# Kernel tuning notes

Measured on AMD Instinct MI355X. Metric: run time of the kernel, lower is better.

## Reference

```python
import jax, jax.numpy as jnp
import numpy as np

N_HEAD = 16


def setup_inputs() -> dict:
    key = jax.random.key(0)
    k1, k2, k3 = jax.random.split(key, 3)
    B, T, C = 4, 2048, 1024
    x = jax.random.normal(k1, (B, T, C), dtype=jnp.float32)
    W = jax.random.normal(k2, (3 * C, C), dtype=jnp.float32) * (1.0 / np.sqrt(C))
    b = jax.random.normal(k3, (3 * C,), dtype=jnp.float32) * 0.02
    return {"x": x, "W": W, "b": b, "input_pos": 0}


def reference(x, W, b, input_pos):
    # cache=False path; input_pos is unused (kept for signature fidelity).
    B, T, C = x.shape
    H = N_HEAD
    hs = C // H
    # Fused QKV projection: torch Linear is x @ W.T + b -> [B, T, 3C]
    qkv = (jnp.einsum('btc,oc->bto', x, W) + b).reshape(B, T, 3, H, hs)
    # q, k, v: [B, H, T, hs]
    q = jnp.transpose(qkv[:, :, 0], (0, 2, 1, 3))
    k = jnp.transpose(qkv[:, :, 1], (0, 2, 1, 3))
    v = jnp.transpose(qkv[:, :, 2], (0, 2, 1, 3))
    scale = hs ** (-0.5)
    # scores: [B, H, T, T]
    scores = jnp.einsum('bhqd,bhkd->bhqk', q, k) * scale
    causal = jnp.tril(jnp.ones((T, T), dtype=bool))
    scores = jnp.where(causal, scores, -jnp.inf)
    wei = jax.nn.softmax(scores, axis=-1)
    out = jnp.einsum('bhqk,bhkd->bhqd', wei, v)  # [B, H, T, hs]
    return jnp.transpose(out, (0, 2, 1, 3)).reshape(B, T, C)
```

## Files before the change

### kernel.cpp

```cpp
#include <hip/hip_runtime.h>
#include <stdint.h>

using s16x8 = __attribute__((ext_vector_type(8))) short;
using u16x8 = __attribute__((ext_vector_type(8))) unsigned short;
using f32x4 = __attribute__((ext_vector_type(4))) float;

#define NEG_INF (-__builtin_inff())

__device__ __forceinline__ unsigned short f2bf(float f) {
    union { float f; uint32_t u; } v; v.f = f;
    uint32_t u = (v.u + 0x7FFFu + ((v.u >> 16) & 1u)) >> 16;
    return (unsigned short)u;
}

__device__ __forceinline__ f32x4 zero4() { f32x4 z = {0.f, 0.f, 0.f, 0.f}; return z; }

__device__ __forceinline__ void async16(const void* g, void* l) {
    __builtin_amdgcn_global_load_lds(
        reinterpret_cast<const uint32_t __attribute__((address_space(1)))*>(
            reinterpret_cast<uintptr_t>(g)),
        reinterpret_cast<uint32_t __attribute__((address_space(3)))*>(
            (uint32_t)reinterpret_cast<uintptr_t>(l)),
        16, 0, 0);
}

__global__ void cvt_bf16(const float* __restrict__ in, unsigned short* __restrict__ out, int n) {
    int i = (blockIdx.x * 256 + threadIdx.x) * 8;
    if (i >= n) return;
    f32x4 a = *(const f32x4*)(in + i);
    f32x4 c = *(const f32x4*)(in + i + 4);
    u16x8 o;
    o[0] = f2bf(a[0]); o[1] = f2bf(a[1]); o[2] = f2bf(a[2]); o[3] = f2bf(a[3]);
    o[4] = f2bf(c[0]); o[5] = f2bf(c[1]); o[6] = f2bf(c[2]); o[7] = f2bf(c[3]);
    *(u16x8*)(out + i) = o;
}

__global__ __launch_bounds__(256, 2)
void qkv_gemm(const unsigned short* __restrict__ A,
              const unsigned short* __restrict__ Bw,
              const float* __restrict__ bias,
              unsigned short* __restrict__ Qo,
              unsigned short* __restrict__ Ko,
              unsigned short* __restrict__ Vto) {
    constexpr int Kd = 1024, T = 2048, H = 16;
    __shared__ __align__(16) unsigned short As[128 * 64];
    __shared__ __align__(16) unsigned short Bs[128 * 64];
    const int tid = threadIdx.x;
    const int wave = tid >> 6, lane = tid & 63;
    const int q4 = lane >> 4, l15 = lane & 15;
    const int bm = blockIdx.y * 128, bn = blockIdx.x * 128;
    const int wm = (wave >> 1) * 64, wn = (wave & 1) * 64;

    f32x4 acc[4][4];
#pragma unroll
    for (int a = 0; a < 4; ++a)
#pragma unroll
        for (int c = 0; c < 4; ++c) acc[a][c] = zero4();

    for (int k0 = 0; k0 < Kd; k0 += 64) {
#pragma unroll
        for (int r = 0; r < 4; ++r) {
            int u = r * 256 + tid;
            int row = u >> 3, su = (u & 7) ^ (row & 7);
            async16(A + (size_t)(bm + row) * Kd + k0 + su * 8, (char*)As + u * 16);
        }
#pragma unroll
        for (int r = 0; r < 4; ++r) {
            int u = r * 256 + tid;
            int row = u >> 3, su = (u & 7) ^ (row & 7);
            async16(Bw + (size_t)(bn + row) * Kd + k0 + su * 8, (char*)Bs + u * 16);
        }
        __syncthreads();
#pragma unroll
        for (int kt = 0; kt < 2; ++kt) {
            s16x8 af[4];
#pragma unroll
            for (int mt = 0; mt < 4; ++mt) {
                int row = wm + mt * 16 + l15;
                int uu = (kt * 4 + q4) ^ (row & 7);
                af[mt] = *(const s16x8*)(As + row * 64 + uu * 8);
            }
#pragma unroll
            for (int nt = 0; nt < 4; ++nt) {
                int row = wn + nt * 16 + l15;
                int uu = (kt * 4 + q4) ^ (row & 7);
                s16x8 bfv = *(const s16x8*)(Bs + row * 64 + uu * 8);
#pragma unroll
                for (int mt = 0; mt < 4; ++mt)
                    acc[mt][nt] = __builtin_amdgcn_mfma_f32_16x16x32_bf16(af[mt], bfv, acc[mt][nt], 0, 0, 0);
            }
        }
        __syncthreads();
    }
#pragma unroll
    for (int nt = 0; nt < 4; ++nt) {
        int n = bn + wn + nt * 16 + l15;
        float bv = bias[n];
        int which = n >> 10, h = (n >> 6) & (H - 1), d = n & 63;
        if (which == 2) {
#pragma unroll
            for (int mt = 0; mt < 4; ++mt)
#pragma unroll
                for (int i = 0; i < 4; ++i) {
                    int m = bm + wm + mt * 16 + 4 * q4 + i;
                    int bb = m >> 11, t = m & (T - 1);
                    Vto[(((size_t)(bb * H + h)) * 64 + d) * T + t] = f2bf(acc[mt][nt][i] + bv);
                }
        } else {
            unsigned short* dst = (which == 0) ? Qo : Ko;
#pragma unroll
            for (int mt = 0; mt < 4; ++mt)
#pragma unroll
                for (int i = 0; i < 4; ++i) {
                    int m = bm + wm + mt * 16 + 4 * q4 + i;
                    int bb = m >> 11, t = m & (T - 1);
                    dst[((((size_t)bb * H + h) * T) + t) * 64 + d] = f2bf(acc[mt][nt][i] + bv);
                }
        }
    }
}

#define SC 0.18033688011112042f
__global__ __launch_bounds__(256, 2)
void flash_attn(const unsigned short* __restrict__ Qg,
                const unsigned short* __restrict__ Kg,
                const unsigned short* __restrict__ Vtg,
                float* __restrict__ Out) {
    constexpr int T = 2048;
    __shared__ __align__(16) unsigned short Qs[128 * 64];
    __shared__ __align__(16) unsigned short Ks[64 * 64];
    __shared__ __align__(16) unsigned short Vt[64 * 64];
    __shared__ __align__(16) unsigned short Ps[4][2][16 * 72];

    const int tid = threadIdx.x;
    const int wave = tid >> 6, lane = tid & 63;
    const int q4 = lane >> 4, l15 = lane & 15;
    const int bh = blockIdx.x;
    const int qt = (int)gridDim.y - 1 - (int)blockIdx.y;
    const int b = bh >> 4, h = bh & 15;
    const int q0 = qt * 128;
    const unsigned short* qb = Qg + (size_t)bh * T * 64;
    const unsigned short* kb = Kg + (size_t)bh * T * 64;
    const unsigned short* vtb = Vtg + (size_t)bh * 64 * T;

#pragma unroll
    for (int r = 0; r < 4; ++r) {
        int u = r * 256 + tid;
        int row = u >> 3, su = (u & 7) ^ (row & 7);
        async16(qb + (size_t)(q0 + row) * 64 + su * 8, (char*)Qs + u * 16);
    }
    __syncthreads();
    s16x8 aq[2][2];
#pragma unroll
    for (int s = 0; s < 2; ++s)
#pragma unroll
        for (int kt = 0; kt < 2; ++kt) {
            int arow = s * 64 + wave * 16 + l15;
            int au = (kt * 4 + q4) ^ (arow & 7);
            aq[s][kt] = *(const s16x8*)(Qs + arow * 64 + au * 8);
        }

    f32x4 oacc[2][4];
    float lsum[2][4];
#pragma unroll
    for (int s = 0; s < 2; ++s) {
#pragma unroll
        for (int ct = 0; ct < 4; ++ct) oacc[s][ct] = zero4();
#pragma unroll
        for (int i = 0; i < 4; ++i) lsum[s][i] = 0.f;
    }

    const int nkt = 2 * qt + 2;
    for (int j = 0; j < nkt; ++j) {
        const int c0 = j * 64;
#pragma unroll
        for (int r = 0; r < 2; ++r) {
            int u = r * 256 + tid;
            int row = u >> 3, su = (u & 7) ^ (row & 7);
            async16(kb + (size_t)(c0 + row) * 64 + su * 8, (char*)Ks + u * 16);
        }
#pragma unroll
        for (int r = 0; r < 2; ++r) {
            int u = r * 256 + tid;
            int row = u >> 3, su = (u & 7) ^ (row & 7);
            async16(vtb + (size_t)row * T + c0 + su * 8, (char*)Vt + u * 16);
        }
        __syncthreads();

#pragma unroll
        for (int s = 0; s < 2; ++s) {
            const int mode = 2 * qt + s - j;
            if (mode < 0) continue;

            f32x4 sv[4];
#pragma unroll
            for (int t = 0; t < 4; ++t) sv[t] = zero4();
#pragma unroll
            for (int kt = 0; kt < 2; ++kt) {
#pragma unroll
                for (int t = 0; t < 4; ++t) {
                    int brow = t * 16 + l15;
                    int bu = (kt * 4 + q4) ^ (brow & 7);
                    s16x8 bk = *(const s16x8*)(Ks + brow * 64 + bu * 8);
                    sv[t] = __builtin_amdgcn_mfma_f32_16x16x32_bf16(aq[s][kt], bk, sv[t], 0, 0, 0);
                }
            }
#pragma unroll
            for (int t = 0; t < 4; ++t) {
#pragma unroll
                for (int i = 0; i < 4; ++i) {
                    float p = exp2f(fmaf(sv[t][i], SC, -16.f));
                    if (mode == 0) {
                        int col = c0 + t * 16 + l15;
                        int row = q0 + s * 64 + wave * 16 + 4 * q4 + i;
                        if (col > row) p = 0.f;
                    }
                    lsum[s][i] += p;
                    union { float f; uint32_t u; } pb; pb.f = p;
                    Ps[wave][s][(4 * q4 + i) * 72 + t * 16 + l15] =
                        (unsigned short)((pb.u + 0x8000u) >> 16);
                }
            }
#pragma unroll
            for (int kt = 0; kt < 2; ++kt) {
                s16x8 pa = *(const s16x8*)(&Ps[wave][s][l15 * 72 + kt * 32 + q4 * 8]);
#pragma unroll
                for (int ct = 0; ct < 4; ++ct) {
                    int vrow = ct * 16 + l15;
                    int vu = (kt * 4 + q4) ^ (vrow & 7);
                    s16x8 vv = *(const s16x8*)(Vt + vrow * 64 + vu * 8);
                    oacc[s][ct] = __builtin_amdgcn_mfma_f32_16x16x32_bf16(pa, vv, oacc[s][ct], 0, 0, 0);
                }
            }
        }
        __syncthreads();
    }
#pragma unroll
    for (int s = 0; s < 2; ++s) {
        float inv[4];
#pragma unroll
        for (int i = 0; i < 4; ++i) {
            float rs = lsum[s][i];
            rs += __shfl_xor(rs, 1, 16);
            rs += __shfl_xor(rs, 2, 16);
            rs += __shfl_xor(rs, 4, 16);
            rs += __shfl_xor(rs, 8, 16);
            inv[i] = 1.0f / rs;
        }
#pragma unroll
        for (int ct = 0; ct < 4; ++ct)
#pragma unroll
            for (int i = 0; i < 4; ++i) {
                int row = q0 + s * 64 + wave * 16 + 4 * q4 + i;
                Out[((size_t)b * T + row) * 1024 + h * 64 + ct * 16 + l15] =
                    oacc[s][ct][i] * inv[i];
            }
    }
}

extern "C" void kernel_launch(void* const* d_in, const int* in_sizes, int n_in,
                              void* d_out, int out_size, void* d_ws, size_t ws_size,
                              hipStream_t stream) {
    const float* x = (const float*)d_in[0];
    const float* W = (const float*)d_in[1];
    const float* bias = (const float*)d_in[2];
    float* out = (float*)d_out;

    unsigned short* xb = (unsigned short*)d_ws;
    unsigned short* wb = xb + 8388608;
    unsigned short* qb = wb + 3145728;
    unsigned short* kb = qb + 8388608;
    unsigned short* vtb = kb + 8388608;

    cvt_bf16<<<dim3(8388608 / 2048), dim3(256), 0, stream>>>(x, xb, 8388608);
    cvt_bf16<<<dim3(3145728 / 2048), dim3(256), 0, stream>>>(W, wb, 3145728);
    qkv_gemm<<<dim3(24, 64), dim3(256), 0, stream>>>(xb, wb, bias, qb, kb, vtb);
    flash_attn<<<dim3(64, 16), dim3(256), 0, stream>>>(qb, kb, vtb, out);
}
```

Measured before the change: 225.0 us.

## Fold softmax scale into Q, reuse Q LDS for P, share K fragments across halves

Moves the softmax scale multiply into the QKV GEMM epilogue so Q is stored prescaled, leaving a bare exp2 in attention. Reuses the Q shared-memory buffer (dead once Q sits in registers) as the P staging area with an XOR-swizzled layout, removing the separate Ps allocation. The attention kernel's launch bound goes to 4 blocks per CU. Each K fragment is now loaded once and used for both 64-row halves, and the PV MFMAs are interleaved. The larger score working set and higher occupancy target may cause register spills. The fixed -16 exponent offset is also dropped, so exp2 is now computed without any max subtraction.

```diff
diff --git a/kernel.cpp b/kernel.cpp
--- a/kernel.cpp
+++ b/kernel.cpp
@@ -4,8 +4,6 @@
 using s16x8 = __attribute__((ext_vector_type(8))) short;
 using u16x8 = __attribute__((ext_vector_type(8))) unsigned short;
 using f32x4 = __attribute__((ext_vector_type(4))) float;
-
-#define NEG_INF (-__builtin_inff())
 
 __device__ __forceinline__ unsigned short f2bf(float f) {
     union { float f; uint32_t u; } v; v.f = f;
@@ -34,6 +32,8 @@
     o[4] = f2bf(c[0]); o[5] = f2bf(c[1]); o[6] = f2bf(c[2]); o[7] = f2bf(c[3]);
     *(u16x8*)(out + i) = o;
 }
+
+#define SC 0.18033688011112042f
 
 __global__ __launch_bounds__(256, 2)
 void qkv_gemm(const unsigned short* __restrict__ A,
@@ -108,20 +108,20 @@
                 }
         } else {
             unsigned short* dst = (which == 0) ? Qo : Ko;
+            float scl = (which == 0) ? SC : 1.0f;
 #pragma unroll
             for (int mt = 0; mt < 4; ++mt)
 #pragma unroll
                 for (int i = 0; i < 4; ++i) {
                     int m = bm + wm + mt * 16 + 4 * q4 + i;
                     int bb = m >> 11, t = m & (T - 1);
-                    dst[((((size_t)bb * H + h) * T) + t) * 64 + d] = f2bf(acc[mt][nt][i] + bv);
+                    dst[((((size_t)bb * H + h) * T) + t) * 64 + d] = f2bf((acc[mt][nt][i] + bv) * scl);
                 }
         }
     }
 }
 
-#define SC 0.18033688011112042f
-__global__ __launch_bounds__(256, 2)
+__global__ __launch_bounds__(256, 4)
 void flash_attn(const unsigned short* __restrict__ Qg,
                 const unsigned short* __restrict__ Kg,
                 const unsigned short* __restrict__ Vtg,
@@ -130,7 +130,6 @@
     __shared__ __align__(16) unsigned short Qs[128 * 64];
     __shared__ __align__(16) unsigned short Ks[64 * 64];
     __shared__ __align__(16) unsigned short Vt[64 * 64];
-    __shared__ __align__(16) unsigned short Ps[4][2][16 * 72];
 
     const int tid = threadIdx.x;
     const int wave = tid >> 6, lane = tid & 63;
@@ -159,6 +158,8 @@
             int au = (kt * 4 + q4) ^ (arow & 7);
             aq[s][kt] = *(const s16x8*)(Qs + arow * 64 + au * 8);
         }
+    unsigned short* const Ps0 = Qs + (wave * 2 + 0) * 1024;
+    unsigned short* const Ps1 = Qs + (wave * 2 + 1) * 1024;
 
     f32x4 oacc[2][4];
     float lsum[2][4];
@@ -187,50 +188,66 @@
         }
         __syncthreads();
 
+        const bool alive0 = (j <= 2 * qt);
+        const bool diag0 = (j == 2 * qt);
+        const bool diag1 = (j == 2 * qt + 1);
+
+        f32x4 sv[2][4];
+#pragma unroll
+        for (int s = 0; s < 2; ++s)
+#pragma unroll
+            for (int t = 0; t < 4; ++t) sv[s][t] = zero4();
+#pragma unroll
+        for (int kt = 0; kt < 2; ++kt) {
+#pragma unroll
+            for (int t = 0; t < 4; ++t) {
+                int brow = t * 16 + l15;
+                int bu = (kt * 4 + q4) ^ (brow & 7);
+                s16x8 bk = *(const s16x8*)(Ks + brow * 64 + bu * 8);
+                sv[0][t] = __builtin_amdgcn_mfma_f32_16x16x32_bf16(aq[0][kt], bk, sv[0][t], 0, 0, 0);
+                sv[1][t] = __builtin_amdgcn_mfma_f32_16x16x32_bf16(aq[1][kt], bk, sv[1][t], 0, 0, 0);
+            }
+        }
+
 #pragma unroll
         for (int s = 0; s < 2; ++s) {
-            const int mode = 2 * qt + s - j;
-            if (mode < 0) continue;
-
-            f32x4 sv[4];
-#pragma unroll
-            for (int t = 0; t < 4; ++t) sv[t] = zero4();
-#pragma unroll
-            for (int kt = 0; kt < 2; ++kt) {
-#pragma unroll
-                for (int t = 0; t < 4; ++t) {
-                    int brow = t * 16 + l15;
-                    int bu = (kt * 4 + q4) ^ (brow & 7);
-                    s16x8 bk = *(const s16x8*)(Ks + brow * 64 + bu * 8);
-                    sv[t] = __builtin_amdgcn_mfma_f32_16x16x32_bf16(aq[s][kt], bk, sv[t], 0, 0, 0);
-                }
-            }
+            if (s == 0 && !alive0) continue;
+            const bool dg = (s == 0) ? diag0 : diag1;
+            unsigned short* const ps = (s == 0) ? Ps0 : Ps1;
 #pragma unroll
             for (int t = 0; t < 4; ++t) {
 #pragma unroll
                 for (int i = 0; i < 4; ++i) {
-                    float p = exp2f(fmaf(sv[t][i], SC, -16.f));
-                    if (mode == 0) {
+                    float p = exp2f(sv[s][t][i]);
+                    if (dg) {
                         int col = c0 + t * 16 + l15;
                         int row = q0 + s * 64 + wave * 16 + 4 * q4 + i;
                         if (col > row) p = 0.f;
                     }
                     lsum[s][i] += p;
                     union { float f; uint32_t u; } pb; pb.f = p;
-                    Ps[wave][s][(4 * q4 + i) * 72 + t * 16 + l15] =
+                    int prow = 4 * q4 + i;
+                    int unit = (t * 2 + (l15 >> 3)) ^ (prow & 7);
+                    ps[prow * 64 + unit * 8 + (l15 & 7)] =
                         (unsigned short)((pb.u + 0x8000u) >> 16);
                 }
             }
-#pragma unroll
-            for (int kt = 0; kt < 2; ++kt) {
-                s16x8 pa = *(const s16x8*)(&Ps[wave][s][l15 * 72 + kt * 32 + q4 * 8]);
-#pragma unroll
-                for (int ct = 0; ct < 4; ++ct) {
-                    int vrow = ct * 16 + l15;
-                    int vu = (kt * 4 + q4) ^ (vrow & 7);
-                    s16x8 vv = *(const s16x8*)(Vt + vrow * 64 + vu * 8);
-                    oacc[s][ct] = __builtin_amdgcn_mfma_f32_16x16x32_bf16(pa, vv, oacc[s][ct], 0, 0, 0);
-                }
+        }
+
+#pragma unroll
+        for (int kt = 0; kt < 2; ++kt) {
+            int pu = ((kt * 4 + q4) ^ (l15 & 7)) * 8;
+            s16x8 pa0, pa1;
+            if (alive0) pa0 = *(const s16x8*)(Ps0 + l15 * 64 + pu);
+            pa1 = *(const s16x8*)(Ps1 + l15 * 64 + pu);
+#pragma unroll
+            for (int ct = 0; ct < 4; ++ct) {
+                int vrow = ct * 16 + l15;
+                int vu = (kt * 4 + q4) ^ (vrow & 7);
+                s16x8 vv = *(const s16x8*)(Vt + vrow * 64 + vu * 8);
+                if (alive0)
+                    oacc[0][ct] = __builtin_amdgcn_mfma_f32_16x16x32_bf16(pa0, vv, oacc[0][ct], 0, 0, 0);
+                oacc[1][ct] = __builtin_amdgcn_mfma_f32_16x16x32_bf16(pa1, vv, oacc[1][ct], 0, 0, 0);
             }
         }
         __syncthreads();
```

Result: slower. 346.1 us (+53.8%).
